# Kernel tuning notes

Hardware: AMD Instinct MI355X
Metric: run time of the kernel (lower is better)

## Reference

```python
import jax, jax.numpy as jnp
import numpy as np

NUM_GROUPS = 32
EPS = 1e-6


def group_norm(x, scale, bias):
    # x: (b, c, h, w), affine GroupNorm with 32 groups, eps=1e-6
    b, c, h, w = x.shape
    xg = x.reshape(b, NUM_GROUPS, c // NUM_GROUPS, h, w)
    mean = xg.mean(axis=(2, 3, 4), keepdims=True)
    var = xg.var(axis=(2, 3, 4), keepdims=True)
    xg = (xg - mean) * jax.lax.rsqrt(var + EPS)
    x = xg.reshape(b, c, h, w)
    return x * scale[None, :, None, None] + bias[None, :, None, None]


def conv1x1(x, w, b):
    # 1x1 conv == per-pixel matmul over channels
    return jnp.einsum('bchw,oc->bohw', x, w) + b[None, :, None, None]


def setup_inputs() -> dict:
    key = jax.random.key(0)
    ks = jax.random.split(key, 10)
    B, C, H, W = 4, 512, 64, 64
    x = jax.random.normal(ks[0], (B, C, H, W), dtype=jnp.float32)
    s = 0.02
    return {
        'x': x,
        'gn_scale': jnp.ones((C,), jnp.float32),
        'gn_bias': jnp.zeros((C,), jnp.float32),
        'wq': jax.random.normal(ks[1], (C, C), jnp.float32) * s,
        'bq': jnp.zeros((C,), jnp.float32),
        'wk': jax.random.normal(ks[2], (C, C), jnp.float32) * s,
        'bk': jnp.zeros((C,), jnp.float32),
        'wv': jax.random.normal(ks[3], (C, C), jnp.float32) * s,
        'bv': jnp.zeros((C,), jnp.float32),
        'wp': jax.random.normal(ks[4], (C, C), jnp.float32) * s,
        'bp': jnp.zeros((C,), jnp.float32),
    }


def reference(x, gn_scale, gn_bias, wq, bq, wk, bk, wv, bv, wp, bp):
    # NOTE: the original torch code shadows the residual `h = x` with the
    # integer height from `b, c, h, w = q.shape`, so `return x + h` adds the
    # scalar spatial height, NOT the residual. We replicate that exactly.
    height_scalar = x.shape[2]
    xn = group_norm(x, gn_scale, gn_bias)
    q = conv1x1(xn, wq, bq)
    k = conv1x1(xn, wk, bk)
    v = conv1x1(xn, wv, bv)
    b, c, h, w = q.shape
    hw = h * w
    qf = q.reshape(b, c, hw)
    kf = k.reshape(b, c, hw)
    vf = v.reshape(b, c, hw)
    # scores[b, i, j] = sum_c q[b, c, i] * k[b, c, j], scaled by c^-0.5
    scores = jnp.einsum('bci,bcj->bij', qf, kf) * (float(c) ** -0.5)
    attn = jax.nn.softmax(scores, axis=-1)  # (b, hw, hw)
    # out[b, c, i] = sum_j attn[b, i, j] * v[b, c, j]
    out = jnp.einsum('bij,bcj->bci', attn, vf).reshape(b, c, h, w)
    out = conv1x1(out, wp, bp)
    return out + jnp.asarray(height_scalar, out.dtype)
```

## Files before the change

kernel.cpp:

```cpp
#include <hip/hip_runtime.h>
#include <hip/hip_bf16.h>

typedef __attribute__((ext_vector_type(4))) float f32x4;
typedef __attribute__((ext_vector_type(16))) float f32x16;
typedef unsigned short u16;
typedef unsigned char u8;
typedef unsigned int u32;
typedef long long i64;

#define MFMA32F8(A,B,C) __builtin_amdgcn_mfma_f32_32x32x16_fp8_fp8(A,B,C,0,0,0)

#define GLOAD_LDS16(g, l) \
  __builtin_amdgcn_global_load_lds((const __attribute__((address_space(1))) void*)(g), \
                                   (__attribute__((address_space(3))) void*)(l), 16, 0, 0)

static __device__ __forceinline__ u16 f2bf(float f) {
  __hip_bfloat16 h = __float2bfloat16(f);
  return *reinterpret_cast<u16*>(&h);
}

static __device__ __forceinline__ u8 f2fp8(float f) {
#if __has_builtin(__builtin_amdgcn_cvt_pk_fp8_f32)
  int v = __builtin_amdgcn_cvt_pk_fp8_f32(f, f, 0, false);
  return (u8)(v & 0xff);
#else
  int r;
  asm volatile("v_cvt_pk_fp8_f32 %0, %1, %1" : "=v"(r) : "v"(f));
  return (u8)(r & 0xff);
#endif
}

static __device__ __forceinline__ u32 pk4fp8(float a, float b, float c, float d) {
#if __has_builtin(__builtin_amdgcn_cvt_pk_fp8_f32)
  u32 v = (u32)__builtin_amdgcn_cvt_pk_fp8_f32(a, b, 0, false);
  return (u32)__builtin_amdgcn_cvt_pk_fp8_f32(c, d, (int)v, true);
#else
  int lo, hi;
  asm volatile("v_cvt_pk_fp8_f32 %0, %1, %2" : "=v"(lo) : "v"(a), "v"(b));
  asm volatile("v_cvt_pk_fp8_f32 %0, %1, %2" : "=v"(hi) : "v"(c), "v"(d));
  return ((u32)lo & 0xffffu) | ((u32)hi << 16);
#endif
}

static __device__ __forceinline__ float fp8tof(u8 x) {
  int s = x >> 7, e = (x >> 3) & 15, m = x & 7;
  float v;
  if (e) { u32 bits = ((u32)(e + 120) << 23) | ((u32)m << 20); v = __uint_as_float(bits); }
  else v = (float)m * 0.001953125f;
  return s ? -v : v;
}

static __device__ __forceinline__ i64 mk64(int lo, int hi) {
  union { int2 d; i64 v; } u; u.d.x = lo; u.d.y = hi; return u.v;
}

__global__ __launch_bounds__(256) void gn_stats(const float* __restrict__ x,
                                                float* __restrict__ stats) {
  int bg = blockIdx.x;
  const float* p = x + (size_t)bg * 16 * 4096;
  float s = 0.f, ss = 0.f;
  for (int i = threadIdx.x; i < 16 * 4096 / 4; i += 256) {
    float4 v = ((const float4*)p)[i];
    s  += v.x + v.y + v.z + v.w;
    ss += v.x*v.x + v.y*v.y + v.z*v.z + v.w*v.w;
  }
  #pragma unroll
  for (int off = 32; off; off >>= 1) { s += __shfl_down(s, off); ss += __shfl_down(ss, off); }
  __shared__ float rs[4], rss[4];
  int wid = threadIdx.x >> 6, lane = threadIdx.x & 63;
  if (lane == 0) { rs[wid] = s; rss[wid] = ss; }
  __syncthreads();
  if (threadIdx.x == 0) {
    float S = rs[0]+rs[1]+rs[2]+rs[3], SS = rss[0]+rss[1]+rss[2]+rss[3];
    float mean = S * (1.f/65536.f);
    float var  = SS * (1.f/65536.f) - mean*mean;
    stats[bg*2]   = mean;
    stats[bg*2+1] = rsqrtf(var + 1e-6f);
  }
}

__global__ __launch_bounds__(256) void norm_tr8(const float* __restrict__ x,
                                                const float* __restrict__ stats,
                                                const float* __restrict__ gsc,
                                                const float* __restrict__ gbi,
                                                u8* __restrict__ xn8) {
  __shared__ u16 T[64][66];
  int b = blockIdx.z, c0 = blockIdx.y * 64, p0 = blockIdx.x * 64;
  int t = threadIdx.x;
  {
    int i = t >> 2, part = t & 3;
    int c = c0 + i, g = c >> 4;
    float mean = stats[(b*32+g)*2], rstd = stats[(b*32+g)*2+1];
    float sc = gsc[c] * rstd;
    float bi = gbi[c] - mean * sc;
    const float* src = x + ((size_t)b*512 + c) * 4096 + p0 + part*16;
    #pragma unroll
    for (int v = 0; v < 4; v++) {
      float4 f = *(const float4*)(src + v*4);
      int px = part*16 + v*4;
      T[i][px+0] = f2bf(f.x*sc + bi);
      T[i][px+1] = f2bf(f.y*sc + bi);
      T[i][px+2] = f2bf(f.z*sc + bi);
      T[i][px+3] = f2bf(f.w*sc + bi);
    }
  }
  __syncthreads();
  {
    int j = t >> 2, part = t & 3;
    float f[16];
    #pragma unroll
    for (int u = 0; u < 16; u++)
      f[u] = __uint_as_float((u32)T[part*16 + u][j] << 16);
    u32 d0 = pk4fp8(f[0], f[1], f[2], f[3]);
    u32 d1 = pk4fp8(f[4], f[5], f[6], f[7]);
    u32 d2 = pk4fp8(f[8], f[9], f[10], f[11]);
    u32 d3 = pk4fp8(f[12], f[13], f[14], f[15]);
    *(int4*)(xn8 + ((size_t)b*4096 + p0 + j)*512 + c0 + part*16) =
        make_int4((int)d0, (int)d1, (int)d2, (int)d3);
  }
}

__global__ __launch_bounds__(256) void wcvt8(const float* __restrict__ wq, const float* __restrict__ wk,
                                             const float* __restrict__ wv, const float* __restrict__ wp,
                                             const float* __restrict__ bq, const float* __restrict__ bk,
                                             const float* __restrict__ bv, const float* __restrict__ bp,
                                             u8* __restrict__ w8, float* __restrict__ bcat) {
  int idx = blockIdx.x * 256 + threadIdx.x;
  int m = idx >> 18, r = idx & 262143;
  const float* src = (m==0) ? wq : (m==1) ? wk : (m==2) ? wv : wp;
  w8[idx] = f2fp8(src[r] * 32.f);
  if (idx < 2048) {
    int mm = idx >> 9, rr = idx & 511;
    const float* bs = (mm==0) ? bq : (mm==1) ? bk : (mm==2) ? bv : bp;
    bcat[idx] = bs[rr];
  }
}

__global__ __launch_bounds__(256, 2) void gemm8(
    const u8* __restrict__ A, size_t aStr, const u8* __restrict__ B, size_t bStr,
    const float* __restrict__ bias, int biasRow,
    u8* __restrict__ out8, float* __restrict__ outF,
    float osc, float outAdd, size_t oStr, int N) {
  __shared__ __align__(16) u8 As[2][128][128];
  __shared__ __align__(16) u8 Bs[2][128][128];
  int bz = blockIdx.z;
  const u8* Ab = A + aStr * bz;
  const u8* Bb = B + bStr * bz;
  int m0 = blockIdx.y * 128, n0 = blockIdx.x * 128;
  int t = threadIdx.x, lane = t & 63, wid = t >> 6;
  int wm = (wid & 1) * 64, wn = (wid >> 1) * 64;
  int ln31 = lane & 31, hi = lane >> 5;
  f32x16 acc[2][2] = {};

  auto STG = [&](int buf, int k0) {
    #pragma unroll
    for (int i = 0; i < 4; i++) {
      int r0 = wid*32 + i*8;
      int row = r0 + (lane >> 3), s = lane & 7;
      GLOAD_LDS16(Ab + (size_t)(m0 + row)*512 + k0 + ((s ^ (row & 7)) << 4), &As[buf][r0][0]);
    }
    #pragma unroll
    for (int i = 0; i < 4; i++) {
      int r0 = wid*32 + i*8;
      int row = r0 + (lane >> 3), s = lane & 7;
      GLOAD_LDS16(Bb + (size_t)(n0 + row)*512 + k0 + ((s ^ (row & 7)) << 4), &Bs[buf][r0][0]);
    }
  };

  STG(0, 0);
  #pragma unroll
  for (int kt = 0; kt < 4; kt++) {
    int cur = kt & 1;
    __builtin_amdgcn_s_barrier();
    if (kt + 1 < 4) {
      STG(cur ^ 1, (kt + 1) * 128);
      asm volatile("s_waitcnt vmcnt(8)" ::: "memory");
    } else {
      asm volatile("s_waitcnt vmcnt(0)" ::: "memory");
    }
    __builtin_amdgcn_s_barrier();
    __builtin_amdgcn_s_setprio(1);
    #pragma unroll
    for (int c = 0; c < 8; c++) {
      i64 af[2], bf_[2];
      #pragma unroll
      for (int mt = 0; mt < 2; mt++) {
        int row = wm + mt*32 + ln31;
        af[mt] = *(const i64*)(&As[cur][row][0] + ((c ^ (row & 7)) << 4) + hi*8);
      }
      #pragma unroll
      for (int nt = 0; nt < 2; nt++) {
        int row = wn + nt*32 + ln31;
        bf_[nt] = *(const i64*)(&Bs[cur][row][0] + ((c ^ (row & 7)) << 4) + hi*8);
      }
      acc[0][0] = MFMA32F8(af[0], bf_[0], acc[0][0]);
      acc[0][1] = MFMA32F8(af[0], bf_[1], acc[0][1]);
      acc[1][0] = MFMA32F8(af[1], bf_[0], acc[1][0]);
      acc[1][1] = MFMA32F8(af[1], bf_[1], acc[1][1]);
    }
    __builtin_amdgcn_s_setprio(0);
  }
  #pragma unroll
  for (int mt = 0; mt < 2; mt++) {
    int mb = m0 + wm + mt*32;
    float4 brow[4];
    if (biasRow) {
      #pragma unroll
      for (int g = 0; g < 4; g++) brow[g] = *(const float4*)&bias[mb + g*8 + 4*hi];
    }
    #pragma unroll
    for (int nt = 0; nt < 2; nt++) {
      int gn = n0 + wn + nt*32 + ln31;
      float bn = biasRow ? 0.f : bias[gn];
      #pragma unroll
      for (int r = 0; r < 16; r++) {
        int gm = mb + (r & 3) + 8*(r >> 2) + 4*hi;
        float bb = biasRow ? ((const float*)&brow[r >> 2])[r & 3] : bn;
        float v = acc[mt][nt][r] * osc + bb + outAdd;
        size_t off = oStr * bz + (size_t)gm * N + gn;
        if (outF) outF[off] = v;
        else      out8[off] = f2fp8(v);
      }
    }
  }
}

__global__ __launch_bounds__(512, 2) void attn(const u8* __restrict__ qk8,
                                               const u8* __restrict__ v8,
                                               u8* __restrict__ opart,
                                               float* __restrict__ sml_) {
  constexpr int NT = 32, KB = 64;
  constexpr float C = 0.06376510329f;
  __shared__ __align__(16) u8 SM[157696];
  u8* Ks = SM;
  u8* Vs = SM + 65536;
  u8* Pex = SM + 139264;
  float* Plsum = (float*)(SM + 155648);

  int combo = blockIdx.x & 7, qc = blockIdx.x >> 3;
  int b = combo >> 1, jh = combo & 1;
  int q0 = qc * 128;
  int lane = threadIdx.x & 63, wid = threadIdx.x >> 6;
  int ig = wid & 3, ch = wid >> 2;
  int ln31 = lane & 31, hi = lane >> 5;
  int w8id = ig*2 + ch, wpart = ig*2 + (ch^1);

  const u8* Qb = qk8 + ((size_t)b*4096 + q0 + ig*32 + ln31) * 1024;
  const u8* Kb = qk8 + (size_t)b*4096*1024 + 512 + (size_t)(jh*2048)*1024;
  const u8* Vb = v8  + (size_t)b*512*4096 + jh*2048;

  i64 qf[32];
  #pragma unroll
  for (int c = 0; c < 32; c++) qf[c] = *(const i64*)(Qb + c*16 + hi*8);

  int4 vr0, vr1, vr2, vr3;
  int vcb = wid*64 + (lane >> 2), vso = (lane & 3) * 16;
  auto VLOAD = [&](int tt) {
    const u8* src = Vb + (size_t)tt * KB + vso;
    vr0 = *(const int4*)(src + (size_t)(vcb +  0)*4096);
    vr1 = *(const int4*)(src + (size_t)(vcb + 16)*4096);
    vr2 = *(const int4*)(src + (size_t)(vcb + 32)*4096);
    vr3 = *(const int4*)(src + (size_t)(vcb + 48)*4096);
  };
  auto VWRITE = [&](int buf) {
    u8* d0 = Vs + (size_t)(buf*512 + vcb +  0)*72 + vso;
    u8* d1 = Vs + (size_t)(buf*512 + vcb + 16)*72 + vso;
    u8* d2 = Vs + (size_t)(buf*512 + vcb + 32)*72 + vso;
    u8* d3 = Vs + (size_t)(buf*512 + vcb + 48)*72 + vso;
    *(i64*)(d0) = mk64(vr0.x, vr0.y); *(i64*)(d0+8) = mk64(vr0.z, vr0.w);
    *(i64*)(d1) = mk64(vr1.x, vr1.y); *(i64*)(d1+8) = mk64(vr1.z, vr1.w);
    *(i64*)(d2) = mk64(vr2.x, vr2.y); *(i64*)(d2+8) = mk64(vr2.z, vr2.w);
    *(i64*)(d3) = mk64(vr3.x, vr3.y); *(i64*)(d3+8) = mk64(vr3.z, vr3.w);
  };
  auto KSTAGE = [&](int buf, int tt) {
    #pragma unroll
    for (int i = 0; i < 4; i++) {
      int r0 = wid*8 + i*2;
      int row = r0 + (lane >> 5), s = lane & 31;
      GLOAD_LDS16(Kb + (size_t)(tt*KB + row)*1024 + ((s ^ (row & 7)) << 4),
                  Ks + (size_t)(buf*64 + r0)*512);
    }
  };

  f32x16 oacc[8] = {};
  float lr = 0.f;

  VLOAD(0);
  KSTAGE(0, 0);
  asm volatile("s_waitcnt vmcnt(0)" ::: "memory");
  VWRITE(0);
  VLOAD(1);
  asm volatile("s_waitcnt lgkmcnt(0)" ::: "memory");
  __builtin_amdgcn_s_barrier();

  #pragma unroll 1
  for (int tt = 0; tt < NT; tt++) {
    int cur = tt & 1, pslot = tt & 1;

    f32x16 sacc = {};
    int jrow = ch*32 + ln31;
    const u8* krow = Ks + (size_t)(cur*64 + jrow)*512 + hi*8;
    int jx = (jrow & 7) << 4;
    __builtin_amdgcn_s_setprio(1);
    #pragma unroll
    for (int c = 0; c < 32; c++) {
      i64 kf = *(const i64*)(krow + ((c << 4) ^ jx));
      sacc = MFMA32F8(kf, qf[c], sacc);
    }
    __builtin_amdgcn_s_setprio(0);

    int4 pfr;
    float ls;
    {
      float pe[16];
      #pragma unroll
      for (int r = 0; r < 16; r++) pe[r] = exp2f(sacc[r] * C);
      ls = 0.f;
      #pragma unroll
      for (int r = 0; r < 16; r++) ls += pe[r];
      ls += __shfl_xor(ls, 32);
      u32 A0 = pk4fp8(pe[0], pe[1], pe[2], pe[3]);
      u32 B0 = pk4fp8(pe[4], pe[5], pe[6], pe[7]);
      u32 A1 = pk4fp8(pe[8], pe[9], pe[10], pe[11]);
      u32 B1 = pk4fp8(pe[12], pe[13], pe[14], pe[15]);
      u32 pA0 = (u32)__shfl_xor((int)A0, 32), pB0 = (u32)__shfl_xor((int)B0, 32);
      u32 pA1 = (u32)__shfl_xor((int)A1, 32), pB1 = (u32)__shfl_xor((int)B1, 32);
      pfr = make_int4((int)(hi ? pB0 : A0), (int)(hi ? B0 : pA0),
                      (int)(hi ? pB1 : A1), (int)(hi ? B1 : pA1));
    }
    *(int4*)(Pex + (size_t)((pslot*8 + w8id)*64 + lane)*16) = pfr;
    if (lane < 32) Plsum[(pslot*8 + w8id)*32 + ln31] = ls;

    asm volatile("s_waitcnt vmcnt(0)" ::: "memory");
    asm volatile("s_waitcnt lgkmcnt(0)" ::: "memory");
    __builtin_amdgcn_s_barrier();

    if (tt + 1 < NT) {
      KSTAGE(cur ^ 1, tt + 1);
      VWRITE(cur ^ 1);
      VLOAD(tt + 2 < NT ? tt + 2 : NT - 1);
    }
    int4 pp = *(const int4*)(Pex + (size_t)((pslot*8 + wpart)*64 + lane)*16);
    float lso = Plsum[(pslot*8 + wpart)*32 + ln31];
    lr += ls + lso;

    __builtin_amdgcn_s_setprio(1);
    #pragma unroll
    for (int cb = 0; cb < 8; cb++) {
      int crow = ch*256 + cb*32 + ln31;
      const u8* vr = Vs + (size_t)(cur*512 + crow)*72 + hi*8;
      #pragma unroll
      for (int c = 0; c < 4; c++) {
        i64 vf = *(const i64*)(vr + c*16);
        int4 s4 = ((c >> 1) == ch) ? pfr : pp;
        i64 pf = (c & 1) ? mk64(s4.z, s4.w) : mk64(s4.x, s4.y);
        oacc[cb] = MFMA32F8(vf, pf, oacc[cb]);
      }
    }
    __builtin_amdgcn_s_setprio(0);

    if (tt + 1 < NT) {
      asm volatile("s_waitcnt vmcnt(4)" ::: "memory");
    } else {
      asm volatile("s_waitcnt vmcnt(0)" ::: "memory");
    }
    asm volatile("s_waitcnt lgkmcnt(0)" ::: "memory");
    __builtin_amdgcn_s_barrier();
  }

  if (ch == 0 && lane < 32) {
    int rowg = b*4096 + q0 + ig*32 + ln31;
    ((float2*)sml_)[(size_t)jh*16384 + rowg] = make_float2(0.f, lr);
  }
  float inv32 = 32.f / lr;
  u8* myT = SM + wid * 8704;
  #pragma unroll
  for (int cb = 0; cb < 8; cb++)
    #pragma unroll
    for (int g = 0; g < 4; g++) {
      u32 d = pk4fp8(oacc[cb][g*4+0]*inv32, oacc[cb][g*4+1]*inv32,
                     oacc[cb][g*4+2]*inv32, oacc[cb][g*4+3]*inv32);
      *(u32*)(myT + (size_t)ln31*272 + cb*32 + g*8 + hi*4) = d;
    }
  asm volatile("s_waitcnt lgkmcnt(0)" ::: "memory");
  __builtin_amdgcn_s_barrier();
  {
    size_t base = ((size_t)jh*16384 + (size_t)b*4096 + q0 + ig*32) * 512 + ch*256;
    #pragma unroll
    for (int it = 0; it < 8; it++) {
      int q = it*4 + (lane >> 4);
      int4 v = *(const int4*)(myT + (size_t)q*272 + (lane & 15)*16);
      *(int4*)(opart + base + (size_t)q*512 + (lane & 15)*16) = v;
    }
  }
}

__global__ __launch_bounds__(256) void merge(const u8* __restrict__ opart,
                                             const float* __restrict__ sml_,
                                             u8* __restrict__ ao8) {
  int idx = blockIdx.x * 256 + threadIdx.x;
  int row = idx >> 5;
  int cc = (idx & 31) * 16;
  const float2* sml = (const float2*)sml_;
  float2 s0 = sml[row], s1 = sml[16384 + row];
  float M = fmaxf(s0.x, s1.x);
  float w0 = s0.y * exp2f(s0.x - M), w1 = s1.y * exp2f(s1.x - M);
  float inv = 1.f / (w0 + w1);
  w0 *= inv; w1 *= inv;
  const u8* o0 = opart + (size_t)row*512 + cc;
  const u8* o1 = o0 + (size_t)8388608;
  int4 a = *(const int4*)o0, b = *(const int4*)o1;
  const u8* pa = (const u8*)&a;
  const u8* pb = (const u8*)&b;
  u32 d[4];
  #pragma unroll
  for (int g = 0; g < 4; g++) {
    float v0 = fp8tof(pa[g*4+0])*w0 + fp8tof(pb[g*4+0])*w1;
    float v1 = fp8tof(pa[g*4+1])*w0 + fp8tof(pb[g*4+1])*w1;
    float v2 = fp8tof(pa[g*4+2])*w0 + fp8tof(pb[g*4+2])*w1;
    float v3 = fp8tof(pa[g*4+3])*w0 + fp8tof(pb[g*4+3])*w1;
    d[g] = pk4fp8(v0, v1, v2, v3);
  }
  *(int4*)(ao8 + (size_t)row*512 + cc) = make_int4((int)d[0], (int)d[1], (int)d[2], (int)d[3]);
}

extern "C" void kernel_launch(void* const* d_in, const int* in_sizes, int n_in,
                              void* d_out, int out_size, void* d_ws, size_t ws_size,
                              hipStream_t stream) {
  const float* x   = (const float*)d_in[0];
  const float* gsc = (const float*)d_in[1];
  const float* gbi = (const float*)d_in[2];
  const float* wq  = (const float*)d_in[3];
  const float* bq  = (const float*)d_in[4];
  const float* wk  = (const float*)d_in[5];
  const float* bk  = (const float*)d_in[6];
  const float* wv  = (const float*)d_in[7];
  const float* bv  = (const float*)d_in[8];
  const float* wp  = (const float*)d_in[9];
  const float* bp  = (const float*)d_in[10];
  float* out = (float*)d_out;

  char* ws = (char*)d_ws;
  u8*    xn8   = (u8*)(ws);
  u8*    ao8   = (u8*)(ws);
  u8*    qk8   = (u8*)(ws + 8388608);
  u8*    v8    = (u8*)(ws + 25165824);
  u8*    w8    = (u8*)(ws + 33554432);
  float* bcat  = (float*)(ws + 34603008);
  float* stats = (float*)(ws + 34611200);
  float* sml   = (float*)(ws + 34612224);
  u8*    opart = (u8*)(ws + 34874368);

  gn_stats<<<128, 256, 0, stream>>>(x, stats);
  norm_tr8<<<dim3(64, 8, 4), 256, 0, stream>>>(x, stats, gsc, gbi, xn8);
  wcvt8<<<4096, 256, 0, stream>>>(wq, wk, wv, wp, bq, bk, bv, bp, w8, bcat);

  gemm8<<<dim3(8, 32, 4), 256, 0, stream>>>(xn8, (size_t)2097152, w8, (size_t)0,
                                            bcat, 0, qk8, nullptr,
                                            0.03125f, 0.f, (size_t)4194304, 1024);
  gemm8<<<dim3(32, 4, 4), 256, 0, stream>>>(w8 + 1024*512, (size_t)0, xn8, (size_t)2097152,
                                            bcat + 1024, 1, v8, nullptr,
                                            0.03125f, 0.f, (size_t)2097152, 4096);

  attn<<<256, 512, 0, stream>>>(qk8, v8, opart, sml);
  merge<<<2048, 256, 0, stream>>>(opart, sml, ao8);

  gemm8<<<dim3(32, 4, 4), 256, 0, stream>>>(w8 + 1536*512, (size_t)0, ao8, (size_t)2097152,
                                            bcat + 1536, 1, nullptr, out,
                                            0.0009765625f, 64.f, (size_t)2097152, 4096);
}
```

Baseline: 398.9 us.

## Single-buffer fp8 GEMM for higher occupancy and stage fp8 outputs through LDS

```diff
diff --git a/kernel.cpp b/kernel.cpp
--- a/kernel.cpp
+++ b/kernel.cpp
@@ -136,13 +136,16 @@
   }
 }
 
-__global__ __launch_bounds__(256, 2) void gemm8(
-    const u8* __restrict__ A, size_t aStr, const u8* __restrict__ B, size_t bStr,
-    const float* __restrict__ bias, int biasRow,
+template<int BIASM, int OUT8>
+__global__ __launch_bounds__(256, 4) void gemm8s(
+    const u8* __restrict__ A, size_t aStr,
+    const u8* __restrict__ B, size_t bStr,
+    const float* __restrict__ bias,
     u8* __restrict__ out8, float* __restrict__ outF,
-    float osc, float outAdd, size_t oStr, int N) {
-  __shared__ __align__(16) u8 As[2][128][128];
-  __shared__ __align__(16) u8 Bs[2][128][128];
+    float osc, float outAdd, size_t oStr, int ldOut) {
+  __shared__ __align__(16) u8 SM[32768];
+  u8* As = SM;
+  u8* Bs = SM + 16384;
   int bz = blockIdx.z;
   const u8* Ab = A + aStr * bz;
   const u8* Bb = B + bStr * bz;
@@ -152,33 +155,21 @@
   int ln31 = lane & 31, hi = lane >> 5;
   f32x16 acc[2][2] = {};
 
-  auto STG = [&](int buf, int k0) {
+  int srow = (lane >> 3), sslot = lane & 7;
+  #pragma unroll 1
+  for (int kt = 0; kt < 4; kt++) {
+    __syncthreads();
+    int k0 = kt * 128;
     #pragma unroll
     for (int i = 0; i < 4; i++) {
       int r0 = wid*32 + i*8;
-      int row = r0 + (lane >> 3), s = lane & 7;
-      GLOAD_LDS16(Ab + (size_t)(m0 + row)*512 + k0 + ((s ^ (row & 7)) << 4), &As[buf][r0][0]);
-    }
-    #pragma unroll
-    for (int i = 0; i < 4; i++) {
-      int r0 = wid*32 + i*8;
-      int row = r0 + (lane >> 3), s = lane & 7;
-      GLOAD_LDS16(Bb + (size_t)(n0 + row)*512 + k0 + ((s ^ (row & 7)) << 4), &Bs[buf][r0][0]);
-    }
-  };
-
-  STG(0, 0);
-  #pragma unroll
-  for (int kt = 0; kt < 4; kt++) {
-    int cur = kt & 1;
-    __builtin_amdgcn_s_barrier();
-    if (kt + 1 < 4) {
-      STG(cur ^ 1, (kt + 1) * 128);
-      asm volatile("s_waitcnt vmcnt(8)" ::: "memory");
-    } else {
-      asm volatile("s_waitcnt vmcnt(0)" ::: "memory");
-    }
-    __builtin_amdgcn_s_barrier();
+      int row = r0 + srow;
+      int sw = ((sslot ^ (row & 7)) << 4);
+      GLOAD_LDS16(Ab + (size_t)(m0 + row)*512 + k0 + sw, As + r0*128);
+      GLOAD_LDS16(Bb + (size_t)(n0 + row)*512 + k0 + sw, Bs + r0*128);
+    }
+    asm volatile("s_waitcnt vmcnt(0)" ::: "memory");
+    __syncthreads();
     __builtin_amdgcn_s_setprio(1);
     #pragma unroll
     for (int c = 0; c < 8; c++) {
@@ -186,12 +177,12 @@
       #pragma unroll
       for (int mt = 0; mt < 2; mt++) {
         int row = wm + mt*32 + ln31;
-        af[mt] = *(const i64*)(&As[cur][row][0] + ((c ^ (row & 7)) << 4) + hi*8);
+        af[mt] = *(const i64*)(As + row*128 + ((c ^ (row & 7)) << 4) + hi*8);
       }
       #pragma unroll
       for (int nt = 0; nt < 2; nt++) {
         int row = wn + nt*32 + ln31;
-        bf_[nt] = *(const i64*)(&Bs[cur][row][0] + ((c ^ (row & 7)) << 4) + hi*8);
+        bf_[nt] = *(const i64*)(Bs + row*128 + ((c ^ (row & 7)) << 4) + hi*8);
       }
       acc[0][0] = MFMA32F8(af[0], bf_[0], acc[0][0]);
       acc[0][1] = MFMA32F8(af[0], bf_[1], acc[0][1]);
@@ -200,26 +191,48 @@
     }
     __builtin_amdgcn_s_setprio(0);
   }
-  #pragma unroll
-  for (int mt = 0; mt < 2; mt++) {
-    int mb = m0 + wm + mt*32;
-    float4 brow[4];
-    if (biasRow) {
-      #pragma unroll
-      for (int g = 0; g < 4; g++) brow[g] = *(const float4*)&bias[mb + g*8 + 4*hi];
-    }
-    #pragma unroll
-    for (int nt = 0; nt < 2; nt++) {
-      int gn = n0 + wn + nt*32 + ln31;
-      float bn = biasRow ? 0.f : bias[gn];
-      #pragma unroll
-      for (int r = 0; r < 16; r++) {
-        int gm = mb + (r & 3) + 8*(r >> 2) + 4*hi;
-        float bb = biasRow ? ((const float*)&brow[r >> 2])[r & 3] : bn;
-        float v = acc[mt][nt][r] * osc + bb + outAdd;
-        size_t off = oStr * bz + (size_t)gm * N + gn;
-        if (outF) outF[off] = v;
-        else      out8[off] = f2fp8(v);
+
+  if (OUT8) {
+    __syncthreads();
+    u8* Lt = SM;
+    #pragma unroll
+    for (int mt = 0; mt < 2; mt++) {
+      #pragma unroll
+      for (int nt = 0; nt < 2; nt++) {
+        float bn = BIASM ? 0.f : bias[n0 + wn + nt*32 + ln31];
+        #pragma unroll
+        for (int rg = 0; rg < 4; rg++) {
+          int mloc = wm + mt*32 + 8*rg + 4*hi;
+          float4 bm;
+          if (BIASM) bm = *(const float4*)&bias[m0 + mloc];
+          float v0 = acc[mt][nt][rg*4+0]*osc + (BIASM ? bm.x : bn) + outAdd;
+          float v1 = acc[mt][nt][rg*4+1]*osc + (BIASM ? bm.y : bn) + outAdd;
+          float v2 = acc[mt][nt][rg*4+2]*osc + (BIASM ? bm.z : bn) + outAdd;
+          float v3 = acc[mt][nt][rg*4+3]*osc + (BIASM ? bm.w : bn) + outAdd;
+          *(u32*)(Lt + (size_t)(wn + nt*32 + ln31)*132 + mloc) = pk4fp8(v0, v1, v2, v3);
+        }
+      }
+    }
+    __syncthreads();
+    #pragma unroll
+    for (int pass = 0; pass < 4; pass++) {
+      int n = pass*32 + (t >> 3);
+      int4 v = *(const int4*)(Lt + (size_t)n*132 + (t & 7)*16);
+      *(int4*)(out8 + oStr*bz + (size_t)(n0 + n)*ldOut + m0 + (t & 7)*16) = v;
+    }
+  } else {
+    #pragma unroll
+    for (int mt = 0; mt < 2; mt++) {
+      #pragma unroll
+      for (int nt = 0; nt < 2; nt++) {
+        int gn = n0 + wn + nt*32 + ln31;
+        float bn = BIASM ? 0.f : bias[gn];
+        #pragma unroll
+        for (int r = 0; r < 16; r++) {
+          int gm = m0 + wm + mt*32 + (r & 3) + 8*(r >> 2) + 4*hi;
+          float bb = BIASM ? bias[gm] : bn;
+          outF[oStr*bz + (size_t)gm*ldOut + gn] = acc[mt][nt][r]*osc + bb + outAdd;
+        }
       }
     }
   }
@@ -455,17 +468,18 @@
   norm_tr8<<<dim3(64, 8, 4), 256, 0, stream>>>(x, stats, gsc, gbi, xn8);
   wcvt8<<<4096, 256, 0, stream>>>(wq, wk, wv, wp, bq, bk, bv, bp, w8, bcat);
 
-  gemm8<<<dim3(8, 32, 4), 256, 0, stream>>>(xn8, (size_t)2097152, w8, (size_t)0,
-                                            bcat, 0, qk8, nullptr,
-                                            0.03125f, 0.f, (size_t)4194304, 1024);
-  gemm8<<<dim3(32, 4, 4), 256, 0, stream>>>(w8 + 1024*512, (size_t)0, xn8, (size_t)2097152,
-                                            bcat + 1024, 1, v8, nullptr,
-                                            0.03125f, 0.f, (size_t)2097152, 4096);
+  gemm8s<1,1><<<dim3(32, 8, 4), 256, 0, stream>>>(
+      w8, (size_t)0, xn8, (size_t)2097152, bcat,
+      qk8, nullptr, 0.03125f, 0.f, (size_t)4194304, 1024);
+
+  gemm8s<0,1><<<dim3(4, 32, 4), 256, 0, stream>>>(
+      xn8, (size_t)2097152, w8 + 1024*512, (size_t)0, bcat + 1024,
+      v8, nullptr, 0.03125f, 0.f, (size_t)2097152, 4096);
 
   attn<<<256, 512, 0, stream>>>(qk8, v8, opart, sml);
   merge<<<2048, 256, 0, stream>>>(opart, sml, ao8);
 
-  gemm8<<<dim3(32, 4, 4), 256, 0, stream>>>(w8 + 1536*512, (size_t)0, ao8, (size_t)2097152,
-                                            bcat + 1536, 1, nullptr, out,
-                                            0.0009765625f, 64.f, (size_t)2097152, 4096);
-}
+  gemm8s<1,0><<<dim3(32, 4, 4), 256, 0, stream>>>(
+      w8 + 1536*512, (size_t)0, ao8, (size_t)2097152, bcat + 1536,
+      nullptr, out, 0.0009765625f, 64.f, (size_t)2097152, 4096);
+}
```

New measurement: 387.7 us. -2.8%, faster.
